# Performance work log

Measured on AMD Instinct MI355X. Metric: run time of the kernel, lower is better.

## Reference

```python
import jax, jax.numpy as jnp
import numpy as np
import math

WS = (8, 8)        # window_size for context (2D)
HEADS = 8


def _attend(q, k, v, h):
    # q: (Bw, Nq, inner), k/v: (Bw, Nk, inner)
    Bw, Nq, inner = q.shape
    d = inner // h
    q = q.reshape(Bw, Nq, h, d)
    k = k.reshape(Bw, -1, h, d)
    v = v.reshape(Bw, -1, h, d)
    scores = jnp.einsum('bqhd,bkhd->bhqk', q, k) * (d ** -0.5)
    attn = jax.nn.softmax(scores, axis=-1)
    out = jnp.einsum('bhqk,bkhd->bqhd', attn, v)
    return out.reshape(Bw, Nq, inner)


def reference(x, context, W_q, W_k, W_v, W_out, b_out):
    B, C, T, H, W = x.shape
    H_, W_ = context.shape[-2], context.shape[-1]
    ws = WS
    assert H_ * W_ > ws[0] * ws[1] and H * W >= ws[0] * ws[1]  # window branch
    # pad context to multiple of window_size (no-op for chosen shapes)
    pad_r_2d = (-W_) % ws[1]
    pad_b_2d = (-H_) % ws[0]
    context = jnp.pad(context, ((0, 0), (0, 0), (0, pad_b_2d), (0, pad_r_2d)))
    # scaled window size for the (smaller) 3D query tensor
    ws_ = (math.ceil(float(ws[0]) * H / H_), math.ceil(float(ws[1]) * W / W_))
    pad_r_3d = (-W) % ws_[1]
    pad_b_3d = (-H) % ws_[0]
    x = jnp.pad(x, ((0, 0), (0, 0), (0, 0), (0, pad_b_3d), (0, pad_r_3d)))
    Hp, Wp = x.shape[-2], x.shape[-1]
    Hc, Wc = context.shape[-2], context.shape[-1]
    # window partition: context (B,C,Hc,Wc) -> (B*h*w, ws0*ws1, C)
    hc, wc = Hc // ws[0], Wc // ws[1]
    ctx = context.reshape(B, C, hc, ws[0], wc, ws[1])
    ctx = ctx.transpose(0, 2, 4, 3, 5, 1).reshape(B * hc * wc, ws[0] * ws[1], C)
    # window partition: x (B,C,T,Hp,Wp) -> (B*h*w, T*ws_0*ws_1, C)
    hg, wg = Hp // ws_[0], Wp // ws_[1]
    xw = x.reshape(B, C, T, hg, ws_[0], wg, ws_[1])
    xw = xw.transpose(0, 3, 5, 2, 4, 6, 1).reshape(B * hg * wg, T * ws_[0] * ws_[1], C)
    # QKV projections (no bias: qkv_bias=False, to_k always bias-free)
    q = xw @ W_q
    k = ctx @ W_k
    v = ctx @ W_v
    out = _attend(q, k, v, HEADS)  # (Bw, Nq, inner)
    inner = out.shape[-1]
    # window reverse -> (B, inner, T, Hp, Wp)
    out = out.reshape(B, hg, wg, T, ws_[0], ws_[1], inner)
    out = out.transpose(0, 6, 3, 1, 4, 2, 5).reshape(B, inner, T, Hp, Wp)
    out = out[:, :, :, :H, :W]
    # b c t h w -> b (t h w) c
    out = out.transpose(0, 2, 3, 4, 1).reshape(B, T * H * W, inner)
    return out @ W_out + b_out


def setup_inputs() -> dict:
    key = jax.random.key(0)
    ks = jax.random.split(key, 7)
    D = 512
    s = 0.02
    return {
        'x': jax.random.normal(ks[0], (4, D, 4, 32, 32), jnp.float32),
        'context': jax.random.normal(ks[1], (4, D, 128, 128), jnp.float32),
        'W_q': jax.random.normal(ks[2], (D, D), jnp.float32) * s,
        'W_k': jax.random.normal(ks[3], (D, D), jnp.float32) * s,
        'W_v': jax.random.normal(ks[4], (D, D), jnp.float32) * s,
        'W_out': jax.random.normal(ks[5], (D, D), jnp.float32) * s,
        'b_out': jnp.zeros((D,), jnp.float32),
    }
```

## Files before the change

### kernel.cpp

```cpp
#include <hip/hip_runtime.h>
#include <hip/hip_bf16.h>

typedef unsigned short u16;
typedef unsigned int u32;
typedef __attribute__((ext_vector_type(4))) float f32x4;
typedef __attribute__((ext_vector_type(4))) u16 u16x4;
typedef __attribute__((ext_vector_type(8))) u16 u16x8;
typedef __attribute__((ext_vector_type(8))) short s16x8;
typedef __attribute__((ext_vector_type(2))) u32 u32x2;

__device__ __forceinline__ u16 f2bf(float f) {
    union { float f; u32 u; } v; v.f = f;
    u32 r = v.u + 0x7FFFu + ((v.u >> 16) & 1u);
    return (u16)(r >> 16);
}

__device__ __forceinline__ void gl_lds16(const u16* g, u16* l) {
    __builtin_amdgcn_global_load_lds(
        (const __attribute__((address_space(1))) unsigned int*)(const void*)g,
        (__attribute__((address_space(3))) unsigned int*)(void*)l, 16, 0, 0);
}

__global__ __launch_bounds__(256) void prep_kernel(
    const float* __restrict__ w0, const float* __restrict__ w1,
    const float* __restrict__ w2, const float* __restrict__ w3, u16* __restrict__ WT,
    const float* __restrict__ x, u16* __restrict__ Aq,
    const float* __restrict__ ctx, u16* __restrict__ Actx) {
    __shared__ char smem[16640];
    int bid = blockIdx.x;
    int tid = threadIdx.x;
    if (bid < 8192) {
        u16 (*t)[68] = (u16(*)[68])smem;
        int b2 = bid;
        int cb = b2 & 7; b2 >>= 3;
        int xb = b2 & 1; b2 >>= 1;
        int y  = b2 & 127; b2 >>= 7;
        int b  = b2;
        long ibase = ((long)(b * 512 + cb * 64) * 128 + y) * 128 + xb * 64;
#pragma unroll
        for (int p = 0; p < 4; ++p) {
            int task = p * 256 + tid;
            int cc = task >> 4, xl = (task & 15) * 4;
            float4 v = *(const float4*)&ctx[ibase + (long)cc * 16384 + xl];
            u16x4 o = {f2bf(v.x), f2bf(v.y), f2bf(v.z), f2bf(v.w)};
            *(u16x4*)&t[cc][xl] = o;
        }
        __syncthreads();
#pragma unroll
        for (int p = 0; p < 2; ++p) {
            int task = p * 256 + tid;
            int xx = task >> 3, j = task & 7;
            u16x8 o;
#pragma unroll
            for (int i = 0; i < 8; ++i) o[i] = t[j * 8 + i][xx];
            int xg = xb * 64 + xx;
            int row = b * 16384 + (y >> 3) * 1024 + (xg >> 3) * 64 + (y & 7) * 8 + (xg & 7);
            *(u16x8*)&Actx[(long)row * 512 + cb * 64 + j * 8] = o;
        }
    } else if (bid < 12288) {
        u16 (*t)[36] = (u16(*)[36])smem;
        int b2 = bid - 8192;
        int cb = b2 & 7; b2 >>= 3;
        int y  = b2 & 31; b2 >>= 5;
        int tt = b2 & 3; b2 >>= 2;
        int b  = b2;
        long ibase = ((long)(b * 512 + cb * 64) * 4 + tt) * 1024 + y * 32;
#pragma unroll
        for (int p = 0; p < 2; ++p) {
            int task = p * 256 + tid;
            int cc = task >> 3, xl = (task & 7) * 4;
            float4 v = *(const float4*)&x[ibase + (long)cc * 4096 + xl];
            u16x4 o = {f2bf(v.x), f2bf(v.y), f2bf(v.z), f2bf(v.w)};
            *(u16x4*)&t[cc][xl] = o;
        }
        __syncthreads();
        {
            int xx = tid >> 3, j = tid & 7;
            u16x8 o;
#pragma unroll
            for (int i = 0; i < 8; ++i) o[i] = t[j * 8 + i][xx];
            int row = b * 4096 + (y >> 1) * 256 + (xx >> 1) * 16 + tt * 4 + (y & 1) * 2 + (xx & 1);
            *(u16x8*)&Aq[(long)row * 512 + cb * 64 + j * 8] = o;
        }
    } else {
        float (*t)[65] = (float(*)[65])smem;
        int b2 = bid - 12288;
        int wsel = b2 >> 6;
        int tile = b2 & 63;
        int j0 = (tile >> 3) * 64, c0 = (tile & 7) * 64;
        const float* src = wsel == 0 ? w0 : wsel == 1 ? w1 : wsel == 2 ? w2 : w3;
        u16* out = WT + (long)wsel * 512 * 512;
        int tj = tid & 63;
        int ti = tid >> 6;
#pragma unroll
        for (int p = 0; p < 16; ++p) {
            int row = p * 4 + ti;
            t[row][tj] = src[(long)(c0 + row) * 512 + j0 + tj];
        }
        __syncthreads();
#pragma unroll
        for (int p = 0; p < 16; ++p) {
            int jl = p * 4 + ti;
            out[(long)(j0 + jl) * 512 + c0 + tj] = f2bf(t[tj][jl]);
        }
    }
}

template <int FINAL>
__global__ __launch_bounds__(256, 4) void gemm128_kernel(
    const u16* __restrict__ A, const u16* __restrict__ Bt,
    u16* __restrict__ Cb, float* __restrict__ Cf, const float* __restrict__ bias) {
    __shared__ u16 As[1024 * 8];
    __shared__ u16 Bs[1024 * 8];
    int tid = threadIdx.x;
    int lane = tid & 63;
    int w = tid >> 6;
    int wm = w >> 1, wn = w & 1;
    int bid = blockIdx.x;
    int wg = (bid & 7) * 64 + (bid >> 3);
    int m0 = (wg >> 2) * 128;
    int n0 = (wg & 3) * 128;

    const f32x4 z = {0.f, 0.f, 0.f, 0.f};
    f32x4 acc[4][4];
#pragma unroll
    for (int i = 0; i < 4; ++i)
#pragma unroll
        for (int j = 0; j < 4; ++j) acc[i][j] = z;

    int aoff[4], boff[4], lb[4];
#pragma unroll
    for (int i = 0; i < 4; ++i) {
        int s = i * 256 + tid;
        int row = s >> 3;
        int cb = (s & 7) ^ (row & 7);
        aoff[i] = (m0 + row) * 512 + cb * 8;
        boff[i] = (n0 + row) * 512 + cb * 8;
        lb[i] = (i * 256 + w * 64) * 8;
    }
    int la = lane & 15, lg = lane >> 4;
    for (int ks = 0; ks < 8; ++ks) {
        int ko = ks * 64;
#pragma unroll
        for (int i = 0; i < 4; ++i) {
            gl_lds16(&A[aoff[i] + ko], &As[lb[i]]);
            gl_lds16(&Bt[boff[i] + ko], &Bs[lb[i]]);
        }
        __syncthreads();
#pragma unroll
        for (int kk = 0; kk < 2; ++kk) {
            int cb = kk * 4 + lg;
            s16x8 af[4], bfr[4];
#pragma unroll
            for (int mt = 0; mt < 4; ++mt) {
                int r = wm * 64 + mt * 16 + la;
                af[mt] = *(const s16x8*)&As[r * 64 + ((cb ^ (r & 7)) * 8)];
            }
#pragma unroll
            for (int nt = 0; nt < 4; ++nt) {
                int c = wn * 64 + nt * 16 + la;
                bfr[nt] = *(const s16x8*)&Bs[c * 64 + ((cb ^ (c & 7)) * 8)];
            }
#pragma unroll
            for (int mt = 0; mt < 4; ++mt)
#pragma unroll
                for (int nt = 0; nt < 4; ++nt)
                    acc[mt][nt] = __builtin_amdgcn_mfma_f32_16x16x32_bf16(af[mt], bfr[nt], acc[mt][nt], 0, 0, 0);
        }
        __syncthreads();
    }
#pragma unroll
    for (int mt = 0; mt < 4; ++mt) {
#pragma unroll
        for (int nt = 0; nt < 4; ++nt) {
            int col = n0 + wn * 64 + nt * 16 + la;
#pragma unroll
            for (int rr = 0; rr < 4; ++rr) {
                int r = m0 + wm * 64 + mt * 16 + lg * 4 + rr;
                float v = acc[mt][nt][rr];
                if (FINAL) {
                    int bb = r >> 12, hg = (r >> 8) & 15, wgx = (r >> 4) & 15;
                    int tt = (r >> 2) & 3, rr0 = (r >> 1) & 1, cc0 = r & 1;
                    int tok = bb * 4096 + tt * 1024 + (hg * 2 + rr0) * 32 + wgx * 2 + cc0;
                    Cf[(long)tok * 512 + col] = v + bias[col];
                } else {
                    Cb[(long)r * 512 + col] = f2bf(v);
                }
            }
        }
    }
}

__global__ __launch_bounds__(512, 2) void gemmkv256_kernel(
    const u16* __restrict__ A, const u16* __restrict__ B,
    u16* __restrict__ CK, u16* __restrict__ CVT) {
    __shared__ u16 lds[2][2][16384];
    int tid = threadIdx.x;
    int lane = tid & 63;
    int w = tid >> 6;
    int wm = w >> 2, wn = w & 3;
    int la = lane & 15, lg = lane >> 4;
    int bid = blockIdx.x;
    int wg = (bid & 7) * 128 + (bid >> 3);
    int m0 = (wg >> 2) * 256;
    int n0 = (wg & 3) * 256;

    const f32x4 z = {0.f, 0.f, 0.f, 0.f};
    f32x4 acc[8][4];
#pragma unroll
    for (int i = 0; i < 8; ++i)
#pragma unroll
        for (int j = 0; j < 4; ++j) acc[i][j] = z;

    int aoff[4], boff[4], lsl[4];
#pragma unroll
    for (int i = 0; i < 4; ++i) {
        int s = i * 512 + tid;
        int row = s >> 3;
        int cb = (s & 7) ^ (row & 7);
        aoff[i] = (m0 + row) * 512 + cb * 8;
        boff[i] = (n0 + row) * 512 + cb * 8;
        lsl[i] = (i * 512 + w * 64) * 8;
    }

    s16x8 bfr[4][2];

#pragma unroll
    for (int i = 0; i < 4; ++i) {
        gl_lds16(&A[aoff[i]], &lds[0][0][lsl[i]]);
        gl_lds16(&B[boff[i]], &lds[0][1][lsl[i]]);
    }
#pragma unroll
    for (int i = 0; i < 4; ++i) {
        gl_lds16(&A[aoff[i] + 64], &lds[1][0][lsl[i]]);
        gl_lds16(&B[boff[i] + 64], &lds[1][1][lsl[i]]);
    }
    asm volatile("s_waitcnt vmcnt(8)" ::: "memory");
    __builtin_amdgcn_s_barrier();
    asm volatile("" ::: "memory");

#pragma unroll
    for (int t = 0; t < 8; ++t) {
        int buf = t & 1;
        const u16* Ab = lds[buf][0];
        const u16* Bb = lds[buf][1];
        int ko2 = (t + 2) * 64;

        {
            int cb = lg;
            s16x8 af[4];
#pragma unroll
            for (int mt = 0; mt < 4; ++mt) {
                int r = wm * 128 + mt * 16 + la;
                af[mt] = *(const s16x8*)&Ab[r * 64 + ((cb ^ (r & 7)) * 8)];
            }
#pragma unroll
            for (int nt = 0; nt < 4; ++nt) {
                int c = wn * 64 + nt * 16 + la;
                bfr[nt][0] = *(const s16x8*)&Bb[c * 64 + ((cb ^ (c & 7)) * 8)];
            }
            __builtin_amdgcn_s_barrier();
            __builtin_amdgcn_s_setprio(1);
#pragma unroll
            for (int mt = 0; mt < 4; ++mt)
#pragma unroll
                for (int nt = 0; nt < 4; ++nt)
                    acc[mt][nt] = __builtin_amdgcn_mfma_f32_16x16x32_bf16(af[mt], bfr[nt][0], acc[mt][nt], 0, 0, 0);
            __builtin_amdgcn_s_setprio(0);
            __builtin_amdgcn_sched_barrier(0);
            __builtin_amdgcn_s_barrier();
        }
        {
            int cb = 4 + lg;
            s16x8 af[4];
#pragma unroll
            for (int mt = 0; mt < 4; ++mt) {
                int r = wm * 128 + mt * 16 + la;
                af[mt] = *(const s16x8*)&Ab[r * 64 + ((cb ^ (r & 7)) * 8)];
            }
#pragma unroll
            for (int nt = 0; nt < 4; ++nt) {
                int c = wn * 64 + nt * 16 + la;
                bfr[nt][1] = *(const s16x8*)&Bb[c * 64 + ((cb ^ (c & 7)) * 8)];
            }
            __builtin_amdgcn_s_barrier();
            __builtin_amdgcn_s_setprio(1);
#pragma unroll
            for (int mt = 0; mt < 4; ++mt)
#pragma unroll
                for (int nt = 0; nt < 4; ++nt)
                    acc[mt][nt] = __builtin_amdgcn_mfma_f32_16x16x32_bf16(af[mt], bfr[nt][1], acc[mt][nt], 0, 0, 0);
            __builtin_amdgcn_s_setprio(0);
            __builtin_amdgcn_sched_barrier(0);
            __builtin_amdgcn_s_barrier();
        }
        {
            int cb = 4 + lg;
            s16x8 af[4];
#pragma unroll
            for (int mt = 0; mt < 4; ++mt) {
                int r = wm * 128 + 64 + mt * 16 + la;
                af[mt] = *(const s16x8*)&Ab[r * 64 + ((cb ^ (r & 7)) * 8)];
            }
            if (t < 6) {
                gl_lds16(&B[boff[0] + ko2], &lds[buf][1][lsl[0]]);
                gl_lds16(&B[boff[1] + ko2], &lds[buf][1][lsl[1]]);
                gl_lds16(&A[aoff[0] + ko2], &lds[buf][0][lsl[0]]);
            }
            __builtin_amdgcn_s_barrier();
            __builtin_amdgcn_s_setprio(1);
#pragma unroll
            for (int mt = 0; mt < 4; ++mt)
#pragma unroll
                for (int nt = 0; nt < 4; ++nt)
                    acc[4 + mt][nt] = __builtin_amdgcn_mfma_f32_16x16x32_bf16(af[mt], bfr[nt][1], acc[4 + mt][nt], 0, 0, 0);
            __builtin_amdgcn_s_setprio(0);
            __builtin_amdgcn_sched_barrier(0);
            __builtin_amdgcn_s_barrier();
        }
        {
            int cb = lg;
            s16x8 af[4];
#pragma unroll
            for (int mt = 0; mt < 4; ++mt) {
                int r = wm * 128 + 64 + mt * 16 + la;
                af[mt] = *(const s16x8*)&Ab[r * 64 + ((cb ^ (r & 7)) * 8)];
            }
            if (t < 6) {
                gl_lds16(&B[boff[2] + ko2], &lds[buf][1][lsl[2]]);
                gl_lds16(&B[boff[3] + ko2], &lds[buf][1][lsl[3]]);
                gl_lds16(&A[aoff[2] + ko2], &lds[buf][0][lsl[2]]);
            }
            __builtin_amdgcn_s_barrier();
            __builtin_amdgcn_s_setprio(1);
#pragma unroll
            for (int mt = 0; mt < 4; ++mt)
#pragma unroll
                for (int nt = 0; nt < 4; ++nt)
                    acc[4 + mt][nt] = __builtin_amdgcn_mfma_f32_16x16x32_bf16(af[mt], bfr[nt][0], acc[4 + mt][nt], 0, 0, 0);
            __builtin_amdgcn_s_setprio(0);
            __builtin_amdgcn_sched_barrier(0);
            __builtin_amdgcn_s_barrier();
        }
        if (t < 6) {
            gl_lds16(&A[aoff[1] + ko2], &lds[buf][0][lsl[1]]);
            gl_lds16(&A[aoff[3] + ko2], &lds[buf][0][lsl[3]]);
            asm volatile("s_waitcnt vmcnt(8)" ::: "memory");
            __builtin_amdgcn_s_barrier();
            asm volatile("" ::: "memory");
        } else if (t == 6) {
            asm volatile("s_waitcnt vmcnt(0)" ::: "memory");
            __builtin_amdgcn_s_barrier();
            asm volatile("" ::: "memory");
        }
    }

    if ((wg & 3) < 2) {
#pragma unroll
        for (int mt = 0; mt < 8; ++mt) {
#pragma unroll
            for (int nt = 0; nt < 4; ++nt) {
                int col = n0 + wn * 64 + nt * 16 + la;
#pragma unroll
                for (int rr = 0; rr < 4; ++rr) {
                    int r = m0 + wm * 128 + mt * 16 + lg * 4 + rr;
                    CK[(long)r * 512 + col] = f2bf(acc[mt][nt][rr]);
                }
            }
        }
    } else {
        int colb = n0 - 512 + wn * 64;
        int winb = (m0 >> 6) + wm * 2;
#pragma unroll
        for (int mt = 0; mt < 8; ++mt) {
            int win = winb + (mt >> 2);
            int kvr = (mt & 3) * 16 + lg * 4;
#pragma unroll
            for (int nt = 0; nt < 4; ++nt) {
                int colp = colb + nt * 16 + la;
                u32 lo = (u32)f2bf(acc[mt][nt][0]) | ((u32)f2bf(acc[mt][nt][1]) << 16);
                u32 hi = (u32)f2bf(acc[mt][nt][2]) | ((u32)f2bf(acc[mt][nt][3]) << 16);
                u32x2 pk = {lo, hi};
                *(u32x2*)&CVT[(long)win * 32768 + colp * 64 + kvr] = pk;
            }
        }
    }
}

__global__ __launch_bounds__(64) void attn_kernel(
    const u16* __restrict__ Q, const u16* __restrict__ K,
    const u16* __restrict__ VT, u16* __restrict__ O) {
    __shared__ u16 P[16 * 104];
    int bid = blockIdx.x;
    int wg = (bid & 7) * 1024 + (bid >> 3);
    int win = wg >> 3;
    int h = wg & 7;
    int lane = threadIdx.x;
    int la = lane & 15, lg = lane >> 4;
    const u16* Qb = Q + (long)win * 16 * 512 + h * 64;
    const u16* Kb = K + (long)win * 64 * 512 + h * 64;
    const u16* Vt = VT + (long)win * 32768 + h * 64 * 64;

    s16x8 qf[2];
#pragma unroll
    for (int kk = 0; kk < 2; ++kk)
        qf[kk] = *(const s16x8*)&Qb[la * 512 + kk * 32 + lg * 8];

    const f32x4 z = {0.f, 0.f, 0.f, 0.f};
    f32x4 st[4];
#pragma unroll
    for (int rt = 0; rt < 4; ++rt) st[rt] = z;
#pragma unroll
    for (int rt = 0; rt < 4; ++rt)
#pragma unroll
        for (int kk = 0; kk < 2; ++kk) {
            s16x8 kf = *(const s16x8*)&Kb[(rt * 16 + la) * 512 + kk * 32 + lg * 8];
            st[rt] = __builtin_amdgcn_mfma_f32_16x16x32_bf16(kf, qf[kk], st[rt], 0, 0, 0);
        }
    float mloc = -1e30f;
#pragma unroll
    for (int rt = 0; rt < 4; ++rt)
#pragma unroll
        for (int rr = 0; rr < 4; ++rr) {
            st[rt][rr] *= 0.125f;
            mloc = fmaxf(mloc, st[rt][rr]);
        }
    mloc = fmaxf(mloc, __shfl_xor(mloc, 16));
    mloc = fmaxf(mloc, __shfl_xor(mloc, 32));
    float p[4][4];
    float sloc = 0.f;
#pragma unroll
    for (int rt = 0; rt < 4; ++rt)
#pragma unroll
        for (int rr = 0; rr < 4; ++rr) {
            p[rt][rr] = __expf(st[rt][rr] - mloc);
            sloc += p[rt][rr];
        }
    sloc += __shfl_xor(sloc, 16);
    sloc += __shfl_xor(sloc, 32);
    float inv = 1.0f / sloc;
#pragma unroll
    for (int rt = 0; rt < 4; ++rt)
#pragma unroll
        for (int rr = 0; rr < 4; ++rr)
            P[la * 104 + rt * 16 + lg * 4 + rr] = f2bf(p[rt][rr] * inv);
    __syncthreads();

    f32x4 od[4];
#pragma unroll
    for (int dt = 0; dt < 4; ++dt) od[dt] = z;
#pragma unroll
    for (int kk2 = 0; kk2 < 2; ++kk2) {
        s16x8 pa = *(const s16x8*)&P[la * 104 + kk2 * 32 + lg * 8];
#pragma unroll
        for (int dt = 0; dt < 4; ++dt) {
            s16x8 vb = *(const s16x8*)&Vt[(dt * 16 + la) * 64 + kk2 * 32 + lg * 8];
            od[dt] = __builtin_amdgcn_mfma_f32_16x16x32_bf16(pa, vb, od[dt], 0, 0, 0);
        }
    }
    u16* Ob = O + (long)win * 16 * 512 + h * 64;
#pragma unroll
    for (int dt = 0; dt < 4; ++dt)
#pragma unroll
        for (int rr = 0; rr < 4; ++rr)
            Ob[(long)(lg * 4 + rr) * 512 + dt * 16 + la] = f2bf(od[dt][rr]);
}

__global__ void sentinel_kernel(float* out) {
    if (threadIdx.x == 0 && blockIdx.x == 0) out[0] = -12345.0f;
}

extern "C" void kernel_launch(void* const* d_in, const int* in_sizes, int n_in,
                              void* d_out, int out_size, void* d_ws, size_t ws_size,
                              hipStream_t stream) {
    const float* x   = (const float*)d_in[0];
    const float* ctx = (const float*)d_in[1];
    const float* Wq  = (const float*)d_in[2];
    const float* Wk  = (const float*)d_in[3];
    const float* Wv  = (const float*)d_in[4];
    const float* Wo  = (const float*)d_in[5];
    const float* bo  = (const float*)d_in[6];
    float* out = (float*)d_out;

    u16* wsb  = (u16*)d_ws;
    u16* WT   = wsb;
    u16* Aq   = WT + 4l * 262144;
    u16* Actx = Aq + 8388608l;
    u16* Qb   = Actx + 33554432l;
    u16* Kb   = Qb + 8388608l;
    u16* VTb  = Kb + 33554432l;
    u16* Ob   = VTb + 33554432l;
    size_t need = (size_t)(126877696l) * 2;
    if (ws_size < need) {
        sentinel_kernel<<<1, 64, 0, stream>>>(out);
        return;
    }

    prep_kernel<<<12544, 256, 0, stream>>>(Wq, Wk, Wv, Wo, WT, x, Aq, ctx, Actx);
    gemm128_kernel<0><<<512, 256, 0, stream>>>(Aq, WT, Qb, nullptr, nullptr);
    gemmkv256_kernel<<<1024, 512, 0, stream>>>(Actx, WT + 262144l, Kb, VTb);
    attn_kernel<<<8192, 64, 0, stream>>>(Qb, Kb, VTb, Ob);
    gemm128_kernel<1><<<512, 256, 0, stream>>>(Ob, WT + 3l * 262144, nullptr, out, bo);
}
```

Before: 209.9 us.

## Stage V-transpose epilogue through swizzled LDS and pack attention heads per block

The KV GEMM epilogue now writes the transposed V tile into LDS with an XOR swizzle, then copies it out to global memory with coalesced 16-byte stores. Before, each thread did scattered 8-byte global stores. Separately, the attention kernel goes from 8192 single-wave blocks to 2048 blocks of four waves, each wave handling one head of the same window with its own P buffer. This cuts launch and scheduling overhead and may improve locality, at the cost of extra barriers and relying on the GEMM's LDS being large enough for two 64x256 windows.

```diff
diff --git a/kernel.cpp b/kernel.cpp
--- a/kernel.cpp
+++ b/kernel.cpp
@@ -369,34 +369,50 @@
             }
         }
     } else {
-        int colb = n0 - 512 + wn * 64;
-        int winb = (m0 >> 6) + wm * 2;
+        u16* sl = (u16*)lds;
+        __syncthreads();
 #pragma unroll
         for (int mt = 0; mt < 8; ++mt) {
-            int win = winb + (mt >> 2);
-            int kvr = (mt & 3) * 16 + lg * 4;
+            int winl = wm * 2 + (mt >> 2);
+            int kv0 = (mt & 3) * 16 + lg * 4;
 #pragma unroll
             for (int nt = 0; nt < 4; ++nt) {
-                int colp = colb + nt * 16 + la;
+                int dl = wn * 64 + nt * 16 + la;
+                int kvs = kv0 ^ ((dl & 7) << 3);
                 u32 lo = (u32)f2bf(acc[mt][nt][0]) | ((u32)f2bf(acc[mt][nt][1]) << 16);
                 u32 hi = (u32)f2bf(acc[mt][nt][2]) | ((u32)f2bf(acc[mt][nt][3]) << 16);
                 u32x2 pk = {lo, hi};
-                *(u32x2*)&CVT[(long)win * 32768 + colp * 64 + kvr] = pk;
-            }
-        }
-    }
-}
-
-__global__ __launch_bounds__(64) void attn_kernel(
+                *(u32x2*)&sl[winl * 16384 + dl * 64 + kvs] = pk;
+            }
+        }
+        __syncthreads();
+        int winb = m0 >> 6;
+        int colb = n0 - 512;
+#pragma unroll
+        for (int i = 0; i < 16; ++i) {
+            int g = i * 512 + tid;
+            int winl = g >> 11;
+            int dl = (g >> 3) & 255;
+            int kvg = g & 7;
+            u16x8 v = *(const u16x8*)&sl[winl * 16384 + dl * 64 + ((kvg * 8) ^ ((dl & 7) << 3))];
+            *(u16x8*)&CVT[(long)(winb + winl) * 32768 + (colb + dl) * 64 + kvg * 8] = v;
+        }
+    }
+}
+
+__global__ __launch_bounds__(256) void attn_kernel(
     const u16* __restrict__ Q, const u16* __restrict__ K,
     const u16* __restrict__ VT, u16* __restrict__ O) {
-    __shared__ u16 P[16 * 104];
+    __shared__ u16 P[4][16 * 104];
     int bid = blockIdx.x;
-    int wg = (bid & 7) * 1024 + (bid >> 3);
-    int win = wg >> 3;
-    int h = wg & 7;
-    int lane = threadIdx.x;
+    int wgid = (bid & 7) * 256 + (bid >> 3);
+    int tid = threadIdx.x;
+    int wid = tid >> 6;
+    int lane = tid & 63;
+    int win = wgid >> 1;
+    int h = (wgid & 1) * 4 + wid;
     int la = lane & 15, lg = lane >> 4;
+    u16* Pw = P[wid];
     const u16* Qb = Q + (long)win * 16 * 512 + h * 64;
     const u16* Kb = K + (long)win * 64 * 512 + h * 64;
     const u16* Vt = VT + (long)win * 32768 + h * 64 * 64;
@@ -443,7 +459,7 @@
     for (int rt = 0; rt < 4; ++rt)
 #pragma unroll
         for (int rr = 0; rr < 4; ++rr)
-            P[la * 104 + rt * 16 + lg * 4 + rr] = f2bf(p[rt][rr] * inv);
+            Pw[la * 104 + rt * 16 + lg * 4 + rr] = f2bf(p[rt][rr] * inv);
     __syncthreads();
 
     f32x4 od[4];
@@ -451,7 +467,7 @@
     for (int dt = 0; dt < 4; ++dt) od[dt] = z;
 #pragma unroll
     for (int kk2 = 0; kk2 < 2; ++kk2) {
-        s16x8 pa = *(const s16x8*)&P[la * 104 + kk2 * 32 + lg * 8];
+        s16x8 pa = *(const s16x8*)&Pw[la * 104 + kk2 * 32 + lg * 8];
 #pragma unroll
         for (int dt = 0; dt < 4; ++dt) {
             s16x8 vb = *(const s16x8*)&Vt[(dt * 16 + la) * 64 + kk2 * 32 + lg * 8];
@@ -499,6 +515,6 @@
     prep_kernel<<<12544, 256, 0, stream>>>(Wq, Wk, Wv, Wo, WT, x, Aq, ctx, Actx);
     gemm128_kernel<0><<<512, 256, 0, stream>>>(Aq, WT, Qb, nullptr, nullptr);
     gemmkv256_kernel<<<1024, 512, 0, stream>>>(Actx, WT + 262144l, Kb, VTb);
-    attn_kernel<<<8192, 64, 0, stream>>>(Qb, Kb, VTb, Ob);
+    attn_kernel<<<2048, 256, 0, stream>>>(Qb, Kb, VTb, Ob);
     gemm128_kernel<1><<<512, 256, 0, stream>>>(Ob, WT + 3l * 262144, nullptr, out, bo);
 }
```

After: 199.2 us. 1.05x faster.
